# Kernel tuning notes

Hardware: AMD Instinct MI355X
Metric: run time of the kernel (lower is better)

## Reference

```python
import jax, jax.numpy as jnp
import numpy as np

LEAKY_SLOPE = 0.2  # tf.nn.leaky_relu default alpha
N_NODES = 50000
N_EDGES = 800000
IN_DIM = 128
OUT_DIM = 64
HEADS = 4
MLP_HID = 256
MLP_OUT = 128


def setup_inputs() -> dict:
    key = jax.random.key(0)
    ks = jax.random.split(key, 10)
    node_embeddings = jax.random.normal(ks[0], (N_NODES, IN_DIM), dtype=jnp.float32)
    src = jax.random.randint(ks[1], (N_EDGES,), 0, N_NODES, dtype=jnp.int32)
    dst = jax.random.randint(ks[2], (N_EDGES,), 0, N_NODES, dtype=jnp.int32)
    # glorot-ish scales
    W_n = jax.random.normal(ks[3], (HEADS, IN_DIM, OUT_DIM), dtype=jnp.float32) * (1.0 / np.sqrt(IN_DIM))
    a_src = jax.random.normal(ks[4], (HEADS, OUT_DIM), dtype=jnp.float32) * (1.0 / np.sqrt(OUT_DIM))
    a_dst = jax.random.normal(ks[5], (HEADS, OUT_DIM), dtype=jnp.float32) * (1.0 / np.sqrt(OUT_DIM))
    mlp_W1 = jax.random.normal(ks[6], (HEADS * OUT_DIM, MLP_HID), dtype=jnp.float32) * (1.0 / np.sqrt(HEADS * OUT_DIM))
    mlp_b1 = jnp.zeros((MLP_HID,), dtype=jnp.float32)
    mlp_W2 = jax.random.normal(ks[7], (MLP_HID, MLP_OUT), dtype=jnp.float32) * (1.0 / np.sqrt(MLP_HID))
    mlp_b2 = jnp.zeros((MLP_OUT,), dtype=jnp.float32)
    return {"node_embeddings": node_embeddings, "src": src, "dst": dst,
            "W_n": W_n, "a_src": a_src, "a_dst": a_dst,
            "mlp_W1": mlp_W1, "mlp_b1": mlp_b1, "mlp_W2": mlp_W2, "mlp_b2": mlp_b2}


def _gat_forward(node_embeddings, src, dst, W_n, a_src, a_dst, mlp_W1, mlp_b1, mlp_W2, mlp_b2):
    N = node_embeddings.shape[0]
    # per-head linear transform: [N, H, D]
    h = jnp.einsum('nc,hcd->nhd', node_embeddings, W_n)
    # decomposed attention scores at node level, gathered per edge
    s_src = jnp.einsum('nhd,hd->nh', h, a_src)          # [N, H]
    s_dst = jnp.einsum('nhd,hd->nh', h, a_dst)          # [N, H]
    e = jax.nn.leaky_relu(s_src[src] + s_dst[dst], negative_slope=LEAKY_SLOPE)  # [E, H]
    # segment softmax over incoming edges of each dst node
    e_max = jax.ops.segment_max(e, dst, num_segments=N)          # [N, H], -inf for empty
    ex = jnp.exp(e - e_max[dst])                                  # [E, H]
    den = jax.ops.segment_sum(ex, dst, num_segments=N)            # [N, H]
    m = h[src]                                                    # [E, H, D] messages
    num = jax.ops.segment_sum(ex[:, :, None] * m, dst, num_segments=N)  # [N, H, D]
    safe_den = jnp.where(den > 0, den, 1.0)
    head_out = jax.nn.relu(num / safe_den[:, :, None])            # [N, H, D]
    concat = head_out.reshape(N, -1)                              # [N, H*D]
    hidden = jax.nn.relu(concat @ mlp_W1 + mlp_b1)
    return hidden @ mlp_W2 + mlp_b2                               # [N, MLP_OUT]


def reference(node_embeddings, src, dst, W_n, a_src, a_dst, mlp_W1, mlp_b1, mlp_W2, mlp_b2):
    return _gat_forward(node_embeddings, src, dst, W_n, a_src, a_dst,
                        mlp_W1, mlp_b1, mlp_W2, mlp_b2)
```

## Files before the change

kernel.cpp:

```cpp
#include <hip/hip_runtime.h>

#define LEAKY 0.2f

typedef __attribute__((ext_vector_type(8))) short short8;
typedef __attribute__((ext_vector_type(4))) float floatx4;
typedef __attribute__((ext_vector_type(8))) unsigned short ushort8_t;

__device__ __forceinline__ float bf2f(unsigned short u) {
    return __uint_as_float(((unsigned)u) << 16);
}
__device__ __forceinline__ unsigned short f2bf(float f) {
    unsigned u = __float_as_uint(f);
    unsigned r = (u + 0x7fffu + ((u >> 16) & 1u)) >> 16;
    return (unsigned short)r;
}
__device__ __forceinline__ float relu_nan(float v) { return v < 0.0f ? 0.0f : v; }

__device__ __forceinline__ void gload_lds16(const void* g, void* l) {
    __builtin_amdgcn_global_load_lds((const __attribute__((address_space(1))) void*)g,
                                     (__attribute__((address_space(3))) void*)l, 16, 0, 0);
}

__global__ void k_fill(float* __restrict__ p, float val, int n) {
    int i = blockIdx.x * blockDim.x + threadIdx.x;
    if (i < n) p[i] = val;
}

__global__ void k_prep(const float* __restrict__ Wn, unsigned short* __restrict__ WnT,
                       const float* __restrict__ W1, unsigned short* __restrict__ W1T,
                       const float* __restrict__ W2, unsigned short* __restrict__ W2T,
                       const int* __restrict__ dst, int* __restrict__ cnt, int E) {
    const int gs = gridDim.x * blockDim.x;
    const int tid = blockIdx.x * blockDim.x + threadIdx.x;
    for (int i = tid; i < 256 * 128; i += gs) {
        int col = i >> 7, k = i & 127;
        int head = col >> 6, d = col & 63;
        WnT[i] = f2bf(Wn[(size_t)head * 8192 + (size_t)k * 64 + d]);
    }
    for (int i = tid; i < 256 * 256; i += gs) {
        int n = i >> 8, k = i & 255;
        W1T[i] = f2bf(W1[(size_t)k * 256 + n]);
    }
    for (int i = tid; i < 128 * 256; i += gs) {
        int n = i >> 8, k = i & 255;
        W2T[i] = f2bf(W2[(size_t)k * 128 + n]);
    }
    for (int i = tid; i < E; i += gs) atomicAdd(cnt + dst[i], 1);
}

__global__ __launch_bounds__(256) void k_scan1(
    const int* __restrict__ cnt, int* __restrict__ rowptr, int* __restrict__ bsum, int N) {
    __shared__ int wtot[4];
    const int lane = threadIdx.x & 63, wave = threadIdx.x >> 6;
    const int i = blockIdx.x * 256 + threadIdx.x;
    int v = (i < N) ? cnt[i] : 0;
    int x = v;
    for (int off = 1; off < 64; off <<= 1) {
        int y = __shfl_up(x, off, 64);
        if (lane >= off) x += y;
    }
    if (lane == 63) wtot[wave] = x;
    __syncthreads();
    int wo = 0;
    for (int wv = 0; wv < wave; ++wv) wo += wtot[wv];
    if (i < N) rowptr[i] = wo + x - v;
    if (threadIdx.x == 255) bsum[blockIdx.x] = wo + x;
}
__global__ void k_scan2(int* __restrict__ bsum, int nb) {
    const int lane = threadIdx.x;
    int carry = 0;
    for (int base = 0; base < nb; base += 64) {
        int i = base + lane;
        int v = (i < nb) ? bsum[i] : 0;
        int x = v;
        for (int off = 1; off < 64; off <<= 1) {
            int y = __shfl_up(x, off, 64);
            if (lane >= off) x += y;
        }
        if (i < nb) bsum[i] = carry + x - v;
        carry += __shfl(x, 63, 64);
    }
}
__global__ void k_scan3(int* __restrict__ rowptr, const int* __restrict__ bsum,
                        int* __restrict__ wcnt, int N, int E) {
    int i = blockIdx.x * blockDim.x + threadIdx.x;
    if (i < N) {
        int v = rowptr[i] + bsum[i >> 8];
        rowptr[i] = v;
        wcnt[i] = v;
    }
    if (i == N) rowptr[N] = E;
}

__global__ void k_scatter(const int* __restrict__ src, const int* __restrict__ dst,
                          int* __restrict__ wcnt, int* __restrict__ esrc, int E) {
    int e = blockIdx.x * blockDim.x + threadIdx.x;
    if (e < E) {
        int pos = atomicAdd(wcnt + dst[e], 1);
        esrc[pos] = src[e];
    }
}

__global__ __launch_bounds__(256) void k_agg(
    const float* __restrict__ s_src, const float* __restrict__ s_dst,
    const unsigned short* __restrict__ h_bf,
    const int* __restrict__ rowptr, const int* __restrict__ esrc,
    unsigned short* __restrict__ concat, int N) {
    const int t = threadIdx.x;
    const int lane = t & 63;
    const int wave = t >> 6;
    const int n = blockIdx.x * 4 + wave;
    if (n >= N) return;

    const int head = lane >> 4;
    const int c0 = lane << 2;
    const int eslot = lane & 15;
    const int hsel = lane & 48;

    const int beg = rowptr[n], end = rowptr[n + 1];
    const float sdst = s_dst[n * 4 + head];
    float num0 = 0, num1 = 0, num2 = 0, num3 = 0, den = 0;

    int sid = 0;
    float sv = 0.0f;
    if (beg < end && eslot < end - beg) {
        sid = esrc[beg + eslot];
        sv = s_src[sid * 4 + head];
    }

    for (int base = beg; base < end; base += 16) {
        const int nn = end - base;
        int sidn = 0;
        float svn = 0.0f;
        if (base + 16 < end) {
            if (eslot < end - (base + 16)) {
                sidn = esrc[base + 16 + eslot];
                svn = s_src[sidn * 4 + head];
            }
        }
        float my_ex = 0.0f;
        if (eslot < nn) {
            float v = sv + sdst;
            v = fmaxf(v, LEAKY * v);
            my_ex = __expf(v);
        }
#pragma unroll
        for (int e = 0; e < 16; ++e) {
            float ex = __shfl(my_ex, hsel | e, 64);
            int s    = __shfl(sid, e, 64);
            ushort4 hv = *(const ushort4*)(h_bf + (size_t)s * 256 + c0);
            num0 += ex * bf2f(hv.x);
            num1 += ex * bf2f(hv.y);
            num2 += ex * bf2f(hv.z);
            num3 += ex * bf2f(hv.w);
            den  += ex;
        }
        sid = sidn; sv = svn;
    }

    const float inv = 1.0f / (den > 0.0f ? den : 1.0f);
    ushort4 o;
    o.x = f2bf(relu_nan(num0 * inv));
    o.y = f2bf(relu_nan(num1 * inv));
    o.z = f2bf(relu_nan(num2 * inv));
    o.w = f2bf(relu_nan(num3 * inv));
    *(ushort4*)(concat + (size_t)n * 256 + c0) = o;
}

template <int K, int MODE, bool AF32>
__global__ __launch_bounds__(256) void k_gemm(
    const void* __restrict__ A, const unsigned short* __restrict__ BT,
    const float* __restrict__ bias, unsigned short* __restrict__ Cb,
    float* __restrict__ Cf, int N, int ldout,
    const float* __restrict__ asrc, const float* __restrict__ adst,
    float* __restrict__ s_src, float* __restrict__ s_dst) {
    __shared__ unsigned short As[128 * 32];
    __shared__ unsigned short Bs[128 * 32];
    const int t = threadIdx.x;
    const int lane = t & 63;
    const int w = t >> 6;
    const int wy = w >> 1, wx = w & 1;
    const int lm = lane & 15, quad = lane >> 4;
    const int row0 = blockIdx.x * 128;
    const int n0 = blockIdx.y * 128;
    const int srow = lane >> 2;
    const int sk = (lane & 3) * 8;

    floatx4 acc[4][4];
    if (MODE == 0) {
#pragma unroll
        for (int mi = 0; mi < 4; ++mi)
#pragma unroll
            for (int ni = 0; ni < 4; ++ni) acc[mi][ni] = (floatx4){0, 0, 0, 0};
    } else {
#pragma unroll
        for (int ni = 0; ni < 4; ++ni) {
            float b = bias[n0 + wx * 64 + ni * 16 + lm];
#pragma unroll
            for (int mi = 0; mi < 4; ++mi) acc[mi][ni] = (floatx4){b, b, b, b};
        }
    }

    for (int k0 = 0; k0 < K; k0 += 32) {
#pragma unroll
        for (int p = 0; p < 2; ++p) {
            int tr = (p * 4 + w) * 16 + srow;
            int ga = row0 + tr; if (ga >= N) ga = N - 1;
            if (AF32) {
                const float* Af = (const float*)A;
                float4 v0 = *(const float4*)(Af + (size_t)ga * K + k0 + sk);
                float4 v1 = *(const float4*)(Af + (size_t)ga * K + k0 + sk + 4);
                short8 pk;
                pk[0] = (short)f2bf(v0.x); pk[1] = (short)f2bf(v0.y);
                pk[2] = (short)f2bf(v0.z); pk[3] = (short)f2bf(v0.w);
                pk[4] = (short)f2bf(v1.x); pk[5] = (short)f2bf(v1.y);
                pk[6] = (short)f2bf(v1.z); pk[7] = (short)f2bf(v1.w);
                *(short8*)(As + (size_t)tr * 32 + sk) = pk;
            } else {
                gload_lds16((const unsigned short*)A + (size_t)ga * K + k0 + sk,
                            (char*)As + (size_t)tr * 64 + sk * 2);
            }
            gload_lds16(BT + (size_t)(n0 + tr) * K + k0 + sk,
                        (char*)Bs + (size_t)tr * 64 + sk * 2);
        }
        __syncthreads();
        short8 af[4], bfr[4];
#pragma unroll
        for (int mi = 0; mi < 4; ++mi)
            af[mi] = *(const short8*)(As + (size_t)(wy * 64 + mi * 16 + lm) * 32 + quad * 8);
#pragma unroll
        for (int ni = 0; ni < 4; ++ni)
            bfr[ni] = *(const short8*)(Bs + (size_t)(wx * 64 + ni * 16 + lm) * 32 + quad * 8);
#pragma unroll
        for (int mi = 0; mi < 4; ++mi)
#pragma unroll
            for (int ni = 0; ni < 4; ++ni)
                acc[mi][ni] = __builtin_amdgcn_mfma_f32_16x16x32_bf16(af[mi], bfr[ni], acc[mi][ni], 0, 0, 0);
        __syncthreads();
    }

#pragma unroll
    for (int mi = 0; mi < 4; ++mi)
#pragma unroll
        for (int ni = 0; ni < 4; ++ni)
#pragma unroll
            for (int q = 0; q < 4; ++q) {
                int r = row0 + wy * 64 + mi * 16 + quad * 4 + q;
                int c = n0 + wx * 64 + ni * 16 + lm;
                if (r < N) {
                    if (MODE == 0)      Cb[(size_t)r * ldout + c] = f2bf(acc[mi][ni][q]);
                    else if (MODE == 1) Cb[(size_t)r * ldout + c] = f2bf(relu_nan(acc[mi][ni][q]));
                    else                Cf[(size_t)r * ldout + c] = acc[mi][ni][q];
                }
            }

    if (MODE == 0) {
        const int head = blockIdx.y * 2 + wx;
        float as[4], ad[4];
#pragma unroll
        for (int ni = 0; ni < 4; ++ni) {
            int d = ni * 16 + lm;
            as[ni] = asrc[head * 64 + d];
            ad[ni] = adst[head * 64 + d];
        }
#pragma unroll
        for (int mi = 0; mi < 4; ++mi)
#pragma unroll
            for (int q = 0; q < 4; ++q) {
                float ps = acc[mi][0][q] * as[0] + acc[mi][1][q] * as[1]
                         + acc[mi][2][q] * as[2] + acc[mi][3][q] * as[3];
                float pd = acc[mi][0][q] * ad[0] + acc[mi][1][q] * ad[1]
                         + acc[mi][2][q] * ad[2] + acc[mi][3][q] * ad[3];
#pragma unroll
                for (int m = 1; m < 16; m <<= 1) {
                    ps += __shfl_xor(ps, m, 64);
                    pd += __shfl_xor(pd, m, 64);
                }
                if (lm == 0) {
                    int r = row0 + wy * 64 + mi * 16 + quad * 4 + q;
                    if (r < N) {
                        s_src[r * 4 + head] = ps;
                        s_dst[r * 4 + head] = pd;
                    }
                }
            }
    }
}

extern "C" void kernel_launch(void* const* d_in, const int* in_sizes, int n_in,
                              void* d_out, int out_size, void* d_ws, size_t ws_size,
                              hipStream_t stream) {
    const float* X    = (const float*)d_in[0];
    const int* src    = (const int*)d_in[1];
    const int* dst    = (const int*)d_in[2];
    const float* Wn   = (const float*)d_in[3];
    const float* Asrc = (const float*)d_in[4];
    const float* Adst = (const float*)d_in[5];
    const float* W1   = (const float*)d_in[6];
    const float* b1   = (const float*)d_in[7];
    const float* W2   = (const float*)d_in[8];
    const float* b2   = (const float*)d_in[9];
    float* out = (float*)d_out;

    const int N = in_sizes[0] / 128;
    const int E = in_sizes[1];
    const int NBS = (N + 255) / 256;
    const int NR = (N + 127) / 128;

    size_t off = 0;
    char* w = (char*)d_ws;
    unsigned short* h_bf = (unsigned short*)(w + off); off += (size_t)N * 256 * 2;
    float* s_src = (float*)(w + off);                  off += (size_t)N * 4 * 4;
    float* s_dst = (float*)(w + off);                  off += (size_t)N * 4 * 4;
    int* cnt     = (int*)(w + off);                    off += (size_t)N * 4;
    int* rowptr  = (int*)(w + off);                    off += ((size_t)(N + 1) * 4 + 15) & ~15ull;
    int* wcnt    = (int*)(w + off);                    off += (size_t)N * 4;
    int* bsum    = (int*)(w + off);                    off += ((size_t)NBS * 4 + 15) & ~15ull;
    int* esrc    = (int*)(w + off);                    off += (size_t)E * 4;
    unsigned short* W1T = (unsigned short*)(w + off);  off += 256 * 256 * 2;
    unsigned short* W2T = (unsigned short*)(w + off);  off += 128 * 256 * 2;
    unsigned short* WnT = (unsigned short*)(w + off);  off += 256 * 128 * 2;
    const size_t required = off;

    if (ws_size < required) {
        k_fill<<<dim3((out_size + 255) / 256), dim3(256), 0, stream>>>(
            out, (float)(ws_size >> 20), out_size);
        return;
    }

    unsigned short* concat = (unsigned short*)d_out;

    hipMemsetAsync(cnt, 0, (size_t)N * sizeof(int), stream);
    k_prep<<<dim3(2048), dim3(256), 0, stream>>>(Wn, WnT, W1, W1T, W2, W2T, dst, cnt, E);
    k_gemm<128, 0, true><<<dim3(NR, 2), dim3(256), 0, stream>>>(
        X, WnT, nullptr, h_bf, nullptr, N, 256, Asrc, Adst, s_src, s_dst);
    k_scan1<<<dim3(NBS), dim3(256), 0, stream>>>(cnt, rowptr, bsum, N);
    k_scan2<<<dim3(1), dim3(64), 0, stream>>>(bsum, NBS);
    k_scan3<<<dim3((N + 256) / 256), dim3(256), 0, stream>>>(rowptr, bsum, wcnt, N, E);
    k_scatter<<<dim3((E + 255) / 256), dim3(256), 0, stream>>>(src, dst, wcnt, esrc, E);
    k_agg<<<dim3((N + 3) / 4), dim3(256), 0, stream>>>(s_src, s_dst, h_bf, rowptr, esrc,
                                                       concat, N);
    k_gemm<256, 1, false><<<dim3(NR, 2), dim3(256), 0, stream>>>(
        concat, W1T, b1, h_bf, nullptr, N, 256, nullptr, nullptr, nullptr, nullptr);
    k_gemm<256, 2, false><<<dim3(NR, 1), dim3(256), 0, stream>>>(
        h_bf, W2T, b2, nullptr, out, N, 128, nullptr, nullptr, nullptr, nullptr);
}
```

Baseline: 299.9 us.

## Fuse the two MLP GEMMs into one kernel with hidden activations kept in LDS

Replaces the templated GEMM with a dedicated first-layer kernel and a new fused MLP kernel. The fused kernel computes the 256-wide hidden layer for a 64-row tile, applies bias and ReLU into LDS, then runs the second GEMM straight from LDS. This removes the global write and re-read of the hidden activation buffer and one kernel launch. In exchange, blocks are smaller and use more LDS, and each block reloads the full W1 and W2 weight tiles.

```diff
diff --git a/kernel.cpp b/kernel.cpp
--- a/kernel.cpp
+++ b/kernel.cpp
@@ -167,11 +167,9 @@
     *(ushort4*)(concat + (size_t)n * 256 + c0) = o;
 }
 
-template <int K, int MODE, bool AF32>
-__global__ __launch_bounds__(256) void k_gemm(
-    const void* __restrict__ A, const unsigned short* __restrict__ BT,
-    const float* __restrict__ bias, unsigned short* __restrict__ Cb,
-    float* __restrict__ Cf, int N, int ldout,
+__global__ __launch_bounds__(256) void k_gemm0(
+    const float* __restrict__ A, const unsigned short* __restrict__ BT,
+    unsigned short* __restrict__ Cb, int N,
     const float* __restrict__ asrc, const float* __restrict__ adst,
     float* __restrict__ s_src, float* __restrict__ s_dst) {
     __shared__ unsigned short As[128 * 32];
@@ -187,40 +185,25 @@
     const int sk = (lane & 3) * 8;
 
     floatx4 acc[4][4];
-    if (MODE == 0) {
-#pragma unroll
-        for (int mi = 0; mi < 4; ++mi)
-#pragma unroll
-            for (int ni = 0; ni < 4; ++ni) acc[mi][ni] = (floatx4){0, 0, 0, 0};
-    } else {
-#pragma unroll
-        for (int ni = 0; ni < 4; ++ni) {
-            float b = bias[n0 + wx * 64 + ni * 16 + lm];
-#pragma unroll
-            for (int mi = 0; mi < 4; ++mi) acc[mi][ni] = (floatx4){b, b, b, b};
-        }
-    }
-
-    for (int k0 = 0; k0 < K; k0 += 32) {
+#pragma unroll
+    for (int mi = 0; mi < 4; ++mi)
+#pragma unroll
+        for (int ni = 0; ni < 4; ++ni) acc[mi][ni] = (floatx4){0, 0, 0, 0};
+
+    for (int k0 = 0; k0 < 128; k0 += 32) {
 #pragma unroll
         for (int p = 0; p < 2; ++p) {
             int tr = (p * 4 + w) * 16 + srow;
             int ga = row0 + tr; if (ga >= N) ga = N - 1;
-            if (AF32) {
-                const float* Af = (const float*)A;
-                float4 v0 = *(const float4*)(Af + (size_t)ga * K + k0 + sk);
-                float4 v1 = *(const float4*)(Af + (size_t)ga * K + k0 + sk + 4);
-                short8 pk;
-                pk[0] = (short)f2bf(v0.x); pk[1] = (short)f2bf(v0.y);
-                pk[2] = (short)f2bf(v0.z); pk[3] = (short)f2bf(v0.w);
-                pk[4] = (short)f2bf(v1.x); pk[5] = (short)f2bf(v1.y);
-                pk[6] = (short)f2bf(v1.z); pk[7] = (short)f2bf(v1.w);
-                *(short8*)(As + (size_t)tr * 32 + sk) = pk;
-            } else {
-                gload_lds16((const unsigned short*)A + (size_t)ga * K + k0 + sk,
-                            (char*)As + (size_t)tr * 64 + sk * 2);
-            }
-            gload_lds16(BT + (size_t)(n0 + tr) * K + k0 + sk,
+            float4 v0 = *(const float4*)(A + (size_t)ga * 128 + k0 + sk);
+            float4 v1 = *(const float4*)(A + (size_t)ga * 128 + k0 + sk + 4);
+            short8 pk;
+            pk[0] = (short)f2bf(v0.x); pk[1] = (short)f2bf(v0.y);
+            pk[2] = (short)f2bf(v0.z); pk[3] = (short)f2bf(v0.w);
+            pk[4] = (short)f2bf(v1.x); pk[5] = (short)f2bf(v1.y);
+            pk[6] = (short)f2bf(v1.z); pk[7] = (short)f2bf(v1.w);
+            *(short8*)(As + (size_t)tr * 32 + sk) = pk;
+            gload_lds16(BT + (size_t)(n0 + tr) * 128 + k0 + sk,
                         (char*)Bs + (size_t)tr * 64 + sk * 2);
         }
         __syncthreads();
@@ -247,44 +230,146 @@
             for (int q = 0; q < 4; ++q) {
                 int r = row0 + wy * 64 + mi * 16 + quad * 4 + q;
                 int c = n0 + wx * 64 + ni * 16 + lm;
+                if (r < N) Cb[(size_t)r * 256 + c] = f2bf(acc[mi][ni][q]);
+            }
+
+    const int head = blockIdx.y * 2 + wx;
+    float as[4], ad[4];
+#pragma unroll
+    for (int ni = 0; ni < 4; ++ni) {
+        int d = ni * 16 + lm;
+        as[ni] = asrc[head * 64 + d];
+        ad[ni] = adst[head * 64 + d];
+    }
+#pragma unroll
+    for (int mi = 0; mi < 4; ++mi)
+#pragma unroll
+        for (int q = 0; q < 4; ++q) {
+            float ps = acc[mi][0][q] * as[0] + acc[mi][1][q] * as[1]
+                     + acc[mi][2][q] * as[2] + acc[mi][3][q] * as[3];
+            float pd = acc[mi][0][q] * ad[0] + acc[mi][1][q] * ad[1]
+                     + acc[mi][2][q] * ad[2] + acc[mi][3][q] * ad[3];
+#pragma unroll
+            for (int m = 1; m < 16; m <<= 1) {
+                ps += __shfl_xor(ps, m, 64);
+                pd += __shfl_xor(pd, m, 64);
+            }
+            if (lm == 0) {
+                int r = row0 + wy * 64 + mi * 16 + quad * 4 + q;
                 if (r < N) {
-                    if (MODE == 0)      Cb[(size_t)r * ldout + c] = f2bf(acc[mi][ni][q]);
-                    else if (MODE == 1) Cb[(size_t)r * ldout + c] = f2bf(relu_nan(acc[mi][ni][q]));
-                    else                Cf[(size_t)r * ldout + c] = acc[mi][ni][q];
+                    s_src[r * 4 + head] = ps;
+                    s_dst[r * 4 + head] = pd;
                 }
             }
-
-    if (MODE == 0) {
-        const int head = blockIdx.y * 2 + wx;
-        float as[4], ad[4];
-#pragma unroll
-        for (int ni = 0; ni < 4; ++ni) {
-            int d = ni * 16 + lm;
-            as[ni] = asrc[head * 64 + d];
-            ad[ni] = adst[head * 64 + d];
-        }
-#pragma unroll
-        for (int mi = 0; mi < 4; ++mi)
+        }
+}
+
+__global__ __launch_bounds__(256) void k_mlp(
+    const unsigned short* __restrict__ concat,
+    const unsigned short* __restrict__ W1T,
+    const float* __restrict__ b1,
+    const unsigned short* __restrict__ W2T,
+    const float* __restrict__ b2,
+    float* __restrict__ outp, int N) {
+    __shared__ unsigned short As[64 * 32];
+    __shared__ unsigned short Bs[256 * 32];
+    __shared__ unsigned short Hs[64 * 264];
+    const int t = threadIdx.x;
+    const int lane = t & 63;
+    const int w = t >> 6;
+    const int lm = lane & 15, quad = lane >> 4;
+    const int row0 = blockIdx.x * 64;
+    const int tr = t >> 2;
+    const int sk = (t & 3) * 8;
+
+    floatx4 acc[4][4];
+#pragma unroll
+    for (int ni = 0; ni < 4; ++ni) {
+        float b = b1[w * 64 + ni * 16 + lm];
+#pragma unroll
+        for (int mi = 0; mi < 4; ++mi) acc[mi][ni] = (floatx4){b, b, b, b};
+    }
+
+    for (int k0 = 0; k0 < 256; k0 += 32) {
+        {
+            int ga = row0 + tr; if (ga >= N) ga = N - 1;
+            gload_lds16(concat + (size_t)ga * 256 + k0 + sk,
+                        (char*)As + (size_t)tr * 64 + sk * 2);
+        }
+#pragma unroll
+        for (int p = 0; p < 4; ++p) {
+            int rn = p * 64 + tr;
+            gload_lds16(W1T + (size_t)rn * 256 + k0 + sk,
+                        (char*)Bs + (size_t)rn * 64 + sk * 2);
+        }
+        __syncthreads();
+        short8 af[4], bfr[4];
+#pragma unroll
+        for (int mi = 0; mi < 4; ++mi)
+            af[mi] = *(const short8*)(As + (size_t)(mi * 16 + lm) * 32 + quad * 8);
+#pragma unroll
+        for (int ni = 0; ni < 4; ++ni)
+            bfr[ni] = *(const short8*)(Bs + (size_t)(w * 64 + ni * 16 + lm) * 32 + quad * 8);
+#pragma unroll
+        for (int mi = 0; mi < 4; ++mi)
+#pragma unroll
+            for (int ni = 0; ni < 4; ++ni)
+                acc[mi][ni] = __builtin_amdgcn_mfma_f32_16x16x32_bf16(af[mi], bfr[ni], acc[mi][ni], 0, 0, 0);
+        __syncthreads();
+    }
+
+#pragma unroll
+    for (int mi = 0; mi < 4; ++mi)
+#pragma unroll
+        for (int ni = 0; ni < 4; ++ni)
 #pragma unroll
             for (int q = 0; q < 4; ++q) {
-                float ps = acc[mi][0][q] * as[0] + acc[mi][1][q] * as[1]
-                         + acc[mi][2][q] * as[2] + acc[mi][3][q] * as[3];
-                float pd = acc[mi][0][q] * ad[0] + acc[mi][1][q] * ad[1]
-                         + acc[mi][2][q] * ad[2] + acc[mi][3][q] * ad[3];
-#pragma unroll
-                for (int m = 1; m < 16; m <<= 1) {
-                    ps += __shfl_xor(ps, m, 64);
-                    pd += __shfl_xor(pd, m, 64);
-                }
-                if (lm == 0) {
-                    int r = row0 + wy * 64 + mi * 16 + quad * 4 + q;
-                    if (r < N) {
-                        s_src[r * 4 + head] = ps;
-                        s_dst[r * 4 + head] = pd;
-                    }
-                }
-            }
-    }
+                int row = mi * 16 + quad * 4 + q;
+                int col = w * 64 + ni * 16 + lm;
+                Hs[row * 264 + col] = f2bf(relu_nan(acc[mi][ni][q]));
+            }
+
+    floatx4 acc2[4][2];
+#pragma unroll
+    for (int ni = 0; ni < 2; ++ni) {
+        float b = b2[w * 32 + ni * 16 + lm];
+#pragma unroll
+        for (int mi = 0; mi < 4; ++mi) acc2[mi][ni] = (floatx4){b, b, b, b};
+    }
+
+    for (int k0 = 0; k0 < 256; k0 += 32) {
+#pragma unroll
+        for (int p = 0; p < 2; ++p) {
+            int rn = p * 64 + tr;
+            gload_lds16(W2T + (size_t)rn * 256 + k0 + sk,
+                        (char*)Bs + (size_t)rn * 64 + sk * 2);
+        }
+        __syncthreads();
+        short8 af[4], bfr[2];
+#pragma unroll
+        for (int mi = 0; mi < 4; ++mi)
+            af[mi] = *(const short8*)(Hs + (size_t)(mi * 16 + lm) * 264 + k0 + quad * 8);
+#pragma unroll
+        for (int ni = 0; ni < 2; ++ni)
+            bfr[ni] = *(const short8*)(Bs + (size_t)(w * 32 + ni * 16 + lm) * 32 + quad * 8);
+#pragma unroll
+        for (int mi = 0; mi < 4; ++mi)
+#pragma unroll
+            for (int ni = 0; ni < 2; ++ni)
+                acc2[mi][ni] = __builtin_amdgcn_mfma_f32_16x16x32_bf16(af[mi], bfr[ni], acc2[mi][ni], 0, 0, 0);
+        __syncthreads();
+    }
+
+#pragma unroll
+    for (int mi = 0; mi < 4; ++mi)
+#pragma unroll
+        for (int ni = 0; ni < 2; ++ni)
+#pragma unroll
+            for (int q = 0; q < 4; ++q) {
+                int r = row0 + mi * 16 + quad * 4 + q;
+                int c = w * 32 + ni * 16 + lm;
+                if (r < N) outp[(size_t)r * 128 + c] = acc2[mi][ni][q];
+            }
 }
 
 extern "C" void kernel_launch(void* const* d_in, const int* in_sizes, int n_in,
@@ -306,6 +391,7 @@
     const int E = in_sizes[1];
     const int NBS = (N + 255) / 256;
     const int NR = (N + 127) / 128;
+    const int NM = (N + 63) / 64;
 
     size_t off = 0;
     char* w = (char*)d_ws;
@@ -332,16 +418,13 @@
 
     hipMemsetAsync(cnt, 0, (size_t)N * sizeof(int), stream);
     k_prep<<<dim3(2048), dim3(256), 0, stream>>>(Wn, WnT, W1, W1T, W2, W2T, dst, cnt, E);
-    k_gemm<128, 0, true><<<dim3(NR, 2), dim3(256), 0, stream>>>(
-        X, WnT, nullptr, h_bf, nullptr, N, 256, Asrc, Adst, s_src, s_dst);
+    k_gemm0<<<dim3(NR, 2), dim3(256), 0, stream>>>(
+        X, WnT, h_bf, N, Asrc, Adst, s_src, s_dst);
     k_scan1<<<dim3(NBS), dim3(256), 0, stream>>>(cnt, rowptr, bsum, N);
     k_scan2<<<dim3(1), dim3(64), 0, stream>>>(bsum, NBS);
     k_scan3<<<dim3((N + 256) / 256), dim3(256), 0, stream>>>(rowptr, bsum, wcnt, N, E);
     k_scatter<<<dim3((E + 255) / 256), dim3(256), 0, stream>>>(src, dst, wcnt, esrc, E);
     k_agg<<<dim3((N + 3) / 4), dim3(256), 0, stream>>>(s_src, s_dst, h_bf, rowptr, esrc,
                                                        concat, N);
-    k_gemm<256, 1, false><<<dim3(NR, 2), dim3(256), 0, stream>>>(
-        concat, W1T, b1, h_bf, nullptr, N, 256, nullptr, nullptr, nullptr, nullptr);
-    k_gemm<256, 2, false><<<dim3(NR, 1), dim3(256), 0, stream>>>(
-        h_bf, W2T, b2, nullptr, out, N, 128, nullptr, nullptr, nullptr, nullptr);
-}
+    k_mlp<<<dim3(NM), dim3(256), 0, stream>>>(concat, W1T, b1, W2T, b2, out, N);
+}
```

Result: no change. 298.1 us (-0.6%).
